# Performance work log

Measured on AMD Instinct MI355X. Metric: run time of the kernel, lower is better.

The kernel has to match this reference:

```python
import jax, jax.numpy as jnp
import numpy as np


def setup_inputs() -> dict:
    key = jax.random.key(0)
    k1, k2 = jax.random.split(key)
    inputs = jax.random.normal(k1, (16, 64, 64, 64), dtype=jnp.float32)  # NCHW, C=embedding_dim
    codebook = jax.random.normal(k2, (1024, 64), dtype=jnp.float32)      # [K, D]
    return {"inputs": inputs, "codebook": codebook}


def reference(inputs, codebook):
    # inputs: [B, C, H, W] -> [B, H, W, C] -> [N, D]
    D = codebook.shape[1]
    x = jnp.transpose(inputs, (0, 2, 3, 1)).reshape(-1, D)  # [N, D]
    distances = (
        jnp.sum(x * x, axis=1, keepdims=True)
        + jnp.sum(codebook * codebook, axis=1)
        - 2.0 * jnp.matmul(x, codebook.T)
    )
    encoding_indices = jnp.argmin(distances, axis=1)[:, None]  # [N, 1]
    return encoding_indices
```

## Files before the change

kernel.cpp:

```cpp
#include <hip/hip_runtime.h>


typedef float f4 __attribute__((ext_vector_type(4)));
typedef short s8v __attribute__((ext_vector_type(8)));
typedef unsigned int u32;
typedef __attribute__((address_space(1))) const u32* gas1;
typedef __attribute__((address_space(3))) u32* las3;

#define D_DIM 64
#define HW    4096
#define ROWS  128
#define INF_  __builtin_inff()
#define MFMA(a,b,c) __builtin_amdgcn_mfma_f32_16x16x32_bf16(a,b,c,0,0,0)

__device__ __forceinline__ unsigned short bf_rne(float f) {
    u32 u = __builtin_bit_cast(u32, f);
    u32 r = u + 0x7fffu + ((u >> 16) & 1u);
    return (unsigned short)(r >> 16);
}
__device__ __forceinline__ float bf_to_f(unsigned short h) {
    u32 u = ((u32)h) << 16;
    return __builtin_bit_cast(float, u);
}
__device__ __forceinline__ void split3(float f, unsigned short& h,
                                       unsigned short& m, unsigned short& l) {
    h = bf_rne(f);
    float f1 = f - bf_to_f(h);
    m = bf_rne(f1);
    float f2 = f1 - bf_to_f(m);
    l = bf_rne(f2);
}
__device__ __forceinline__ s8v pack8(unsigned short a0, unsigned short a1,
                                     unsigned short a2, unsigned short a3,
                                     unsigned short a4, unsigned short a5,
                                     unsigned short a6, unsigned short a7) {
    uint4 u;
    u.x = a0 | ((u32)a1 << 16);
    u.y = a2 | ((u32)a3 << 16);
    u.z = a4 | ((u32)a5 << 16);
    u.w = a6 | ((u32)a7 << 16);
    return __builtin_bit_cast(s8v, u);
}
__device__ __forceinline__ void gl_lds16(const char* g, char* l) {
    __builtin_amdgcn_global_load_lds((gas1)(const void*)g, (las3)(void*)l, 16, 0, 0);
}

__global__ __launch_bounds__(64) void prep_kernel(const float* __restrict__ cb,
                                                  char* __restrict__ wsb) {
    const int blk = blockIdx.x;
    const int lane = threadIdx.x;
    if (blk < 384) {
        const int T = blk / 6;
        const int rem = blk - T * 6;
        const int s = rem / 3;
        const int L = rem - s * 3;
        const int code = T * 16 + (lane & 15);
        const int ch0 = s * 32 + (lane >> 4) * 8;
        const float* src = cb + code * 64 + ch0;
        unsigned short o[8];
#pragma unroll
        for (int j = 0; j < 8; ++j) {
            unsigned short h, m2, l;
            split3(src[j], h, m2, l);
            o[j] = (L == 0) ? h : (L == 1) ? m2 : l;
        }
        uint4 w;
        w.x = o[0] | ((u32)o[1] << 16);
        w.y = o[2] | ((u32)o[3] << 16);
        w.z = o[4] | ((u32)o[5] << 16);
        w.w = o[6] | ((u32)o[7] << 16);
        *(uint4*)(wsb + (size_t)blk * 1024 + lane * 16) = w;
    } else {
        const int k = (blk - 384) * 64 + lane;
        const f4* row = (const f4*)(cb + (size_t)k * 64);
        float sacc = 0.f;
#pragma unroll
        for (int i = 0; i < 16; ++i) {
            f4 v = row[i];
            sacc = fmaf(v.x, v.x, sacc);
            sacc = fmaf(v.y, v.y, sacc);
            sacc = fmaf(v.z, v.z, sacc);
            sacc = fmaf(v.w, v.w, sacc);
        }
        ((float*)(wsb + 384 * 1024))[k] = sacc;
    }
}

#define BUILD_AS(rs, s) {                                                    \
    const float* xr = (const float*)&xs4[wrow + (rs) * 16 + m_][0];          \
    f4 va = *(const f4*)(xr + (s) * 32 + ko);                                \
    f4 vb = *(const f4*)(xr + (s) * 32 + ko + 4);                            \
    unsigned short h0,h1,h2,h3,h4,h5,h6,h7;                                  \
    unsigned short q0,q1,q2,q3,q4,q5,q6,q7;                                  \
    unsigned short l0,l1,l2,l3,l4,l5,l6,l7;                                  \
    split3(-2.f * va.x, h0, q0, l0); split3(-2.f * va.y, h1, q1, l1);        \
    split3(-2.f * va.z, h2, q2, l2); split3(-2.f * va.w, h3, q3, l3);        \
    split3(-2.f * vb.x, h4, q4, l4); split3(-2.f * vb.y, h5, q5, l5);        \
    split3(-2.f * vb.z, h6, q6, l6); split3(-2.f * vb.w, h7, q7, l7);        \
    Ah##rs##s = pack8(h0,h1,h2,h3,h4,h5,h6,h7);                              \
    Am##rs##s = pack8(q0,q1,q2,q3,q4,q5,q6,q7);                              \
    Al##rs##s = pack8(l0,l1,l2,l3,l4,l5,l6,l7);                              \
}

#define STAGE(T, BUF) {                                                      \
    const char* gs = wsb + (size_t)(T) * 6144 + lane16;                      \
    gl_lds16(gs + quarter * 1024, (BUF) + quarter * 1024);                   \
    if (quarter < 2)                                                         \
        gl_lds16(gs + (4 + quarter) * 1024, (BUF) + (4 + quarter) * 1024);   \
}

#define READ6(LP)                                                            \
    Bh0 = *(const s8v*)((LP) + 0);    Bm0 = *(const s8v*)((LP) + 1024);      \
    Bl0 = *(const s8v*)((LP) + 2048); Bh1 = *(const s8v*)((LP) + 3072);      \
    Bm1 = *(const s8v*)((LP) + 4096); Bl1 = *(const s8v*)((LP) + 5120);

#define MTERM(AH, AM, AL, BH, BM, BL, ACC)                                   \
    ACC = MFMA(AH, BH, ACC); ACC = MFMA(AH, BM, ACC);                        \
    ACC = MFMA(AM, BH, ACC); ACC = MFMA(AH, BL, ACC);                        \
    ACC = MFMA(AM, BM, ACC); ACC = MFMA(AL, BH, ACC);

#define COMPUTE24()                                                          \
    MTERM(Ah00, Am00, Al00, Bh0, Bm0, Bl0, a00)                              \
    MTERM(Ah10, Am10, Al10, Bh0, Bm0, Bl0, a10)                              \
    MTERM(Ah01, Am01, Al01, Bh1, Bm1, Bl1, a01)                              \
    MTERM(Ah11, Am11, Al11, Bh1, Bm1, Bl1, a11)

#define UPD(rs, i, SV) {                                                     \
    float v = SV[i] + en;                                                    \
    bool p = (v < best_##rs##_##i);                                          \
    best_##rs##_##i = p ? v : best_##rs##_##i;                               \
    idx_##rs##_##i  = p ? kn : idx_##rs##_##i;                               \
}
#define EPILOG(T) {                                                          \
    const int kn = (T) * 16 + m_;                                            \
    const float en = sEn[kn];                                                \
    f4 s0 = a00 + a01;                                                       \
    f4 s1 = a10 + a11;                                                       \
    UPD(0,0,s0) UPD(0,1,s0) UPD(0,2,s0) UPD(0,3,s0)                          \
    UPD(1,0,s1) UPD(1,1,s1) UPD(1,2,s1) UPD(1,3,s1)                          \
    a00 = (f4){0.f,0.f,0.f,0.f}; a01 = (f4){0.f,0.f,0.f,0.f};                \
    a10 = (f4){0.f,0.f,0.f,0.f}; a11 = (f4){0.f,0.f,0.f,0.f};                \
}

#define BFLY1(rs, i, msk) {                                                  \
    float ov = __shfl_xor(best_##rs##_##i, msk);                             \
    int   oi = __shfl_xor(idx_##rs##_##i,  msk);                             \
    bool p = (ov < best_##rs##_##i) ||                                       \
             (ov == best_##rs##_##i && oi < idx_##rs##_##i);                 \
    best_##rs##_##i = p ? ov : best_##rs##_##i;                              \
    idx_##rs##_##i  = p ? oi : idx_##rs##_##i;                               \
}
#define BFLY_ALL(msk)                                                        \
    BFLY1(0,0,msk) BFLY1(0,1,msk) BFLY1(0,2,msk) BFLY1(0,3,msk)              \
    BFLY1(1,0,msk) BFLY1(1,1,msk) BFLY1(1,2,msk) BFLY1(1,3,msk)

__global__ __launch_bounds__(256, 2) void vq_kernel(const float* __restrict__ x,
                                                    const char* __restrict__ wsb,
                                                    int* __restrict__ out) {
    __shared__ __align__(16) char LDSA[34816];
    __shared__ float sEn[1024];

    const int tid = threadIdx.x;
    const int lane = tid & 63;
    const int quarter = __builtin_amdgcn_readfirstlane(tid >> 6);
    const int m_ = lane & 15;
    const int ko = (lane >> 4) * 8;
    const int lane16 = lane * 16;
    const int wrow = quarter * 32;
    const int n0 = blockIdx.x * ROWS;
    const int b = n0 >> 12;
    const int hw0 = n0 & (HW - 1);

    f4 (*xs4)[17] = (f4(*)[17])(void*)LDSA;
    char* const buf0 = LDSA;
    char* const buf1 = LDSA + 6144;

    const float* enp = (const float*)(wsb + 384 * 1024);
#pragma unroll
    for (int q = 0; q < 4; ++q) sEn[q * 256 + tid] = enp[q * 256 + tid];

#pragma unroll
    for (int pass = 0; pass < 2; ++pass) {
        const int row = lane + pass * 64;
        const float* g = x + ((size_t)b * D_DIM + quarter * 16) * HW + hw0 + row;
        float v[16];
#pragma unroll
        for (int i = 0; i < 16; ++i) v[i] = g[(size_t)i * HW];
#pragma unroll
        for (int j = 0; j < 4; ++j)
            xs4[row][quarter * 4 + j] = (f4){v[4*j], v[4*j+1], v[4*j+2], v[4*j+3]};
    }
    __syncthreads();

    s8v Ah00, Am00, Al00, Ah01, Am01, Al01;
    s8v Ah10, Am10, Al10, Ah11, Am11, Al11;
    BUILD_AS(0,0) BUILD_AS(0,1) BUILD_AS(1,0) BUILD_AS(1,1)
    __syncthreads();

    f4 a00 = (f4){0.f,0.f,0.f,0.f}, a01 = (f4){0.f,0.f,0.f,0.f};
    f4 a10 = (f4){0.f,0.f,0.f,0.f}, a11 = (f4){0.f,0.f,0.f,0.f};
    float best_0_0=INF_, best_0_1=INF_, best_0_2=INF_, best_0_3=INF_;
    float best_1_0=INF_, best_1_1=INF_, best_1_2=INF_, best_1_3=INF_;
    int idx_0_0=0, idx_0_1=0, idx_0_2=0, idx_0_3=0;
    int idx_1_0=0, idx_1_1=0, idx_1_2=0, idx_1_3=0;

    s8v Bh0, Bm0, Bl0, Bh1, Bm1, Bl1;

    STAGE(0, buf0)
    __syncthreads();

#pragma unroll 1
    for (int tt = 0; tt < 32; ++tt) {
        const int t = 2 * tt;
        STAGE(t + 1, buf1)
        READ6(buf0 + lane16)
        COMPUTE24()
        EPILOG(t)
        __syncthreads();
        if (tt != 31) STAGE(t + 2, buf0)
        READ6(buf1 + lane16)
        COMPUTE24()
        EPILOG(t + 1)
        __syncthreads();
    }

    BFLY_ALL(1) BFLY_ALL(2) BFLY_ALL(4) BFLY_ALL(8)

    if (m_ == 0) {
        const int rbase = (lane >> 4) * 4;
#pragma unroll
        for (int i = 0; i < 4; ++i) {
        }
        out[n0 + wrow + 0 * 16 + rbase + 0] = idx_0_0;
        out[n0 + wrow + 0 * 16 + rbase + 1] = idx_0_1;
        out[n0 + wrow + 0 * 16 + rbase + 2] = idx_0_2;
        out[n0 + wrow + 0 * 16 + rbase + 3] = idx_0_3;
        out[n0 + wrow + 1 * 16 + rbase + 0] = idx_1_0;
        out[n0 + wrow + 1 * 16 + rbase + 1] = idx_1_1;
        out[n0 + wrow + 1 * 16 + rbase + 2] = idx_1_2;
        out[n0 + wrow + 1 * 16 + rbase + 3] = idx_1_3;
    }
}

extern "C" void kernel_launch(void* const* d_in, const int* in_sizes, int n_in,
                              void* d_out, int out_size, void* d_ws, size_t ws_size,
                              hipStream_t stream) {
    const float* x  = (const float*)d_in[0];
    const float* cb = (const float*)d_in[1];
    char* wsb = (char*)d_ws;
    int*  out = (int*)d_out;

    prep_kernel<<<dim3(400), dim3(64), 0, stream>>>(cb, wsb);
    vq_kernel<<<dim3(65536 / ROWS), dim3(256), 0, stream>>>(x, wsb, out);
}
```

Before: 110.6 us.

## Fuse codebook bf16 split and norm computation into main VQ kernel

Removes the separate prep kernel that pre-split the codebook into bf16 hi/mid/lo planes and computed codebook norms. Each block now computes the norms itself and loads fp32 codebook tiles, splitting them in registers and writing them to LDS, with the next tile's load issued before the current tile's MFMAs. This saves a kernel launch and the workspace round trip. In exchange all 512 blocks redo the norm and split work, and the async global-to-LDS copies become synchronous VALU work.

```diff
diff --git a/kernel.cpp b/kernel.cpp
--- a/kernel.cpp
+++ b/kernel.cpp
@@ -4,8 +4,6 @@
 typedef float f4 __attribute__((ext_vector_type(4)));
 typedef short s8v __attribute__((ext_vector_type(8)));
 typedef unsigned int u32;
-typedef __attribute__((address_space(1))) const u32* gas1;
-typedef __attribute__((address_space(3))) u32* las3;
 
 #define D_DIM 64
 #define HW    4096
@@ -40,50 +38,6 @@
     u.z = a4 | ((u32)a5 << 16);
     u.w = a6 | ((u32)a7 << 16);
     return __builtin_bit_cast(s8v, u);
-}
-__device__ __forceinline__ void gl_lds16(const char* g, char* l) {
-    __builtin_amdgcn_global_load_lds((gas1)(const void*)g, (las3)(void*)l, 16, 0, 0);
-}
-
-__global__ __launch_bounds__(64) void prep_kernel(const float* __restrict__ cb,
-                                                  char* __restrict__ wsb) {
-    const int blk = blockIdx.x;
-    const int lane = threadIdx.x;
-    if (blk < 384) {
-        const int T = blk / 6;
-        const int rem = blk - T * 6;
-        const int s = rem / 3;
-        const int L = rem - s * 3;
-        const int code = T * 16 + (lane & 15);
-        const int ch0 = s * 32 + (lane >> 4) * 8;
-        const float* src = cb + code * 64 + ch0;
-        unsigned short o[8];
-#pragma unroll
-        for (int j = 0; j < 8; ++j) {
-            unsigned short h, m2, l;
-            split3(src[j], h, m2, l);
-            o[j] = (L == 0) ? h : (L == 1) ? m2 : l;
-        }
-        uint4 w;
-        w.x = o[0] | ((u32)o[1] << 16);
-        w.y = o[2] | ((u32)o[3] << 16);
-        w.z = o[4] | ((u32)o[5] << 16);
-        w.w = o[6] | ((u32)o[7] << 16);
-        *(uint4*)(wsb + (size_t)blk * 1024 + lane * 16) = w;
-    } else {
-        const int k = (blk - 384) * 64 + lane;
-        const f4* row = (const f4*)(cb + (size_t)k * 64);
-        float sacc = 0.f;
-#pragma unroll
-        for (int i = 0; i < 16; ++i) {
-            f4 v = row[i];
-            sacc = fmaf(v.x, v.x, sacc);
-            sacc = fmaf(v.y, v.y, sacc);
-            sacc = fmaf(v.z, v.z, sacc);
-            sacc = fmaf(v.w, v.w, sacc);
-        }
-        ((float*)(wsb + 384 * 1024))[k] = sacc;
-    }
 }
 
 #define BUILD_AS(rs, s) {                                                    \
@@ -102,11 +56,18 @@
     Al##rs##s = pack8(l0,l1,l2,l3,l4,l5,l6,l7);                              \
 }
 
-#define STAGE(T, BUF) {                                                      \
-    const char* gs = wsb + (size_t)(T) * 6144 + lane16;                      \
-    gl_lds16(gs + quarter * 1024, (BUF) + quarter * 1024);                   \
-    if (quarter < 2)                                                         \
-        gl_lds16(gs + (4 + quarter) * 1024, (BUF) + (4 + quarter) * 1024);   \
+#define SPLIT_WRITE(SRC, BUF) {                                              \
+    unsigned short h0,h1,h2,h3, q0,q1,q2,q3, l0,l1,l2,l3;                    \
+    split3((SRC).x, h0, q0, l0); split3((SRC).y, h1, q1, l1);                \
+    split3((SRC).z, h2, q2, l2); split3((SRC).w, h3, q3, l3);                \
+    char* dbase = (BUF) + sidx * 3072 + dlab;                                \
+    uint2 wv;                                                                \
+    wv.x = h0 | ((u32)h1 << 16); wv.y = h2 | ((u32)h3 << 16);                \
+    *(uint2*)(dbase + 0)    = wv;                                            \
+    wv.x = q0 | ((u32)q1 << 16); wv.y = q2 | ((u32)q3 << 16);                \
+    *(uint2*)(dbase + 1024) = wv;                                            \
+    wv.x = l0 | ((u32)l1 << 16); wv.y = l2 | ((u32)l3 << 16);                \
+    *(uint2*)(dbase + 2048) = wv;                                            \
 }
 
 #define READ6(LP)                                                            \
@@ -155,7 +116,7 @@
     BFLY1(1,0,msk) BFLY1(1,1,msk) BFLY1(1,2,msk) BFLY1(1,3,msk)
 
 __global__ __launch_bounds__(256, 2) void vq_kernel(const float* __restrict__ x,
-                                                    const char* __restrict__ wsb,
+                                                    const float* __restrict__ cb,
                                                     int* __restrict__ out) {
     __shared__ __align__(16) char LDSA[34816];
     __shared__ float sEn[1024];
@@ -171,21 +132,39 @@
     const int b = n0 >> 12;
     const int hw0 = n0 & (HW - 1);
 
+    const int code_l = tid >> 4;
+    const int chq = tid & 15;
+    const int sidx = chq >> 3;
+    const int g = (chq >> 1) & 3;
+    const int dlab = (g * 16 + code_l) * 16 + (chq & 1) * 8;
+
     f4 (*xs4)[17] = (f4(*)[17])(void*)LDSA;
     char* const buf0 = LDSA;
     char* const buf1 = LDSA + 6144;
 
-    const float* enp = (const float*)(wsb + 384 * 1024);
-#pragma unroll
-    for (int q = 0; q < 4; ++q) sEn[q * 256 + tid] = enp[q * 256 + tid];
+#pragma unroll
+    for (int q = 0; q < 4; ++q) {
+        const int k = q * 256 + tid;
+        const f4* row = (const f4*)(cb + (size_t)k * 64);
+        float sacc = 0.f;
+#pragma unroll
+        for (int i = 0; i < 16; ++i) {
+            f4 v = row[i];
+            sacc = fmaf(v.x, v.x, sacc);
+            sacc = fmaf(v.y, v.y, sacc);
+            sacc = fmaf(v.z, v.z, sacc);
+            sacc = fmaf(v.w, v.w, sacc);
+        }
+        sEn[k] = sacc;
+    }
 
 #pragma unroll
     for (int pass = 0; pass < 2; ++pass) {
         const int row = lane + pass * 64;
-        const float* g = x + ((size_t)b * D_DIM + quarter * 16) * HW + hw0 + row;
+        const float* gp = x + ((size_t)b * D_DIM + quarter * 16) * HW + hw0 + row;
         float v[16];
 #pragma unroll
-        for (int i = 0; i < 16; ++i) v[i] = g[(size_t)i * HW];
+        for (int i = 0; i < 16; ++i) v[i] = gp[(size_t)i * HW];
 #pragma unroll
         for (int j = 0; j < 4; ++j)
             xs4[row][quarter * 4 + j] = (f4){v[4*j], v[4*j+1], v[4*j+2], v[4*j+3]};
@@ -206,21 +185,33 @@
 
     s8v Bh0, Bm0, Bl0, Bh1, Bm1, Bl1;
 
-    STAGE(0, buf0)
+    const float* const bsrc = cb + (size_t)code_l * 64 + chq * 4;
+
+    {
+        f4 bs = *(const f4*)bsrc;
+        SPLIT_WRITE(bs, buf0)
+    }
     __syncthreads();
 
 #pragma unroll 1
     for (int tt = 0; tt < 32; ++tt) {
         const int t = 2 * tt;
-        STAGE(t + 1, buf1)
-        READ6(buf0 + lane16)
-        COMPUTE24()
-        EPILOG(t)
+        {
+            f4 bs = *(const f4*)(bsrc + (size_t)(t + 1) * 1024);
+            READ6(buf0 + lane16)
+            COMPUTE24()
+            EPILOG(t)
+            SPLIT_WRITE(bs, buf1)
+        }
         __syncthreads();
-        if (tt != 31) STAGE(t + 2, buf0)
-        READ6(buf1 + lane16)
-        COMPUTE24()
-        EPILOG(t + 1)
+        {
+            const int tn = (tt != 31) ? (t + 2) : 0;
+            f4 bs = *(const f4*)(bsrc + (size_t)tn * 1024);
+            READ6(buf1 + lane16)
+            COMPUTE24()
+            EPILOG(t + 1)
+            if (tt != 31) SPLIT_WRITE(bs, buf0)
+        }
         __syncthreads();
     }
 
@@ -228,9 +219,6 @@
 
     if (m_ == 0) {
         const int rbase = (lane >> 4) * 4;
-#pragma unroll
-        for (int i = 0; i < 4; ++i) {
-        }
         out[n0 + wrow + 0 * 16 + rbase + 0] = idx_0_0;
         out[n0 + wrow + 0 * 16 + rbase + 1] = idx_0_1;
         out[n0 + wrow + 0 * 16 + rbase + 2] = idx_0_2;
@@ -247,9 +235,7 @@
                               hipStream_t stream) {
     const float* x  = (const float*)d_in[0];
     const float* cb = (const float*)d_in[1];
-    char* wsb = (char*)d_ws;
     int*  out = (int*)d_out;
 
-    prep_kernel<<<dim3(400), dim3(64), 0, stream>>>(cb, wsb);
-    vq_kernel<<<dim3(65536 / ROWS), dim3(256), 0, stream>>>(x, wsb, out);
-}
+    vq_kernel<<<dim3(65536 / ROWS), dim3(256), 0, stream>>>(x, cb, out);
+}
```

Result: slower. 133.9 us (+21.1%).
